# Kernel optimization log

Hardware: AMD Instinct MI355X
Metric: run time of the kernel (lower is better)

Reference implementation:

```python
import jax, jax.numpy as jnp
import numpy as np

V, D, H, L, B = 30000, 128, 4, 128, 512
HD = D // H  # head dim = 32
NL = 2       # num xLSTM layers


def _layernorm(x, w, b):
    mu = x.mean(-1, keepdims=True)
    var = x.var(-1, keepdims=True)
    return (x - mu) * jax.lax.rsqrt(var + 1e-5) * w + b


def _groupnorm_heads(h, w):
    # GroupNorm with num_groups = H over the channel dim (per-head norm), h: [B,L,D]
    hh = h.reshape(h.shape[0], h.shape[1], H, HD)
    mu = hh.mean(-1, keepdims=True)
    var = hh.var(-1, keepdims=True)
    hh = (hh - mu) * jax.lax.rsqrt(var + 1e-5)
    return hh.reshape(h.shape) * w


def _slstm_block(x, W, R, b, gnw, lnw, lnb):
    # x: [B,L,D]; W: [4,D,D] input gate projections (i,f,z,o); R: [4,H,HD,HD] block-diagonal
    # per-head recurrent weights; b: [4,D]; gnw: [D] groupnorm scale.
    bsz = x.shape[0]
    xn = _layernorm(x, lnw, lnb)
    pre = jnp.einsum('bld,god->lbgo', xn, W) + b  # [L,B,4,D]

    def step(carry, pre_t):
        h, c, n, m = carry  # each [B,D]
        rec = jnp.einsum('bhd,ghde->bghe', h.reshape(bsz, H, HD), R).reshape(bsz, 4, D)
        g = pre_t + rec
        it, ft, zt, ot = g[:, 0], g[:, 1], g[:, 2], g[:, 3]
        # stabilized exponential gating (sLSTM vanilla backend)
        m_new = jnp.maximum(ft + m, it)
        i = jnp.exp(it - m_new)
        f = jnp.exp(ft + m - m_new)
        c_new = f * c + i * jnp.tanh(zt)
        n_new = f * n + i
        h_new = jax.nn.sigmoid(ot) * c_new / n_new
        return (h_new, c_new, n_new, m_new), h_new

    z = jnp.zeros((bsz, D), x.dtype)
    _, hs = jax.lax.scan(step, (z, z, z, z), pre)
    hs = jnp.transpose(hs, (1, 0, 2))  # [B,L,D]
    return x + _groupnorm_heads(hs, gnw)  # residual block


def setup_inputs() -> dict:
    key = jax.random.key(0)
    ks = jax.random.split(key, 10)
    s = lambda k, shape, sc: jax.random.normal(k, shape, jnp.float32) * sc
    return {
        'x_ids': jax.random.randint(ks[0], (B, L), 0, V),
        'emb': s(ks[1], (V, D), 0.02),
        'ln_w': jnp.ones((NL, D), jnp.float32),
        'ln_b': jnp.zeros((NL, D), jnp.float32),
        'Wg': s(ks[2], (NL, 4, D, D), 0.05),
        'Rg': s(ks[3], (NL, 4, H, HD, HD), 0.05),
        'bg': s(ks[4], (NL, 4, D), 0.02),
        'gn_w': jnp.ones((NL, D), jnp.float32),
        'w1': s(ks[5], (64, D), 0.05),
        'b1': jnp.zeros((64,), jnp.float32),
        'w2': s(ks[6], (2, 64), 0.05),
        'b2': jnp.zeros((2,), jnp.float32),
    }


def reference(x_ids, emb, ln_w, ln_b, Wg, Rg, bg, gn_w, w1, b1, w2, b2):
    x = emb[x_ids]  # [B,L,D] embedding lookup
    for l in range(NL):
        x = _slstm_block(x, Wg[l], Rg[l], bg[l], gn_w[l], ln_w[l], ln_b[l])
    pooled = x.mean(axis=1)  # mean over sequence, [B,D]
    hid = jax.nn.relu(pooled @ w1.T + b1)  # dropout is identity at eval
    return hid @ w2.T + b2  # [B,2] logits
```

## Files before the change

kernel.cpp:

```cpp
#include <hip/hip_runtime.h>

typedef _Float16 f16;
typedef unsigned int uint;
typedef f16 f16x2 __attribute__((ext_vector_type(2)));
typedef f16 f16x8 __attribute__((ext_vector_type(8)));
typedef __fp16 h16x2 __attribute__((ext_vector_type(2)));
typedef float f32x4 __attribute__((ext_vector_type(4)));

#define Bn 512
#define Ln 128
#define Dn 128
#define Cn 512

__device__ __forceinline__ float fdot2f(uint a, uint b, float c) {
#if __has_builtin(__builtin_amdgcn_fdot2)
  return __builtin_amdgcn_fdot2(__builtin_bit_cast(f16x2, a),
                                __builtin_bit_cast(f16x2, b), c, false);
#else
  f16x2 av = __builtin_bit_cast(f16x2, a), bv = __builtin_bit_cast(f16x2, b);
  return c + (float)av[0] * (float)bv[0] + (float)av[1] * (float)bv[1];
#endif
}

__device__ __forceinline__ uint pk2(float a, float b) {
#if __has_builtin(__builtin_amdgcn_cvt_pkrtz)
  h16x2 v = __builtin_amdgcn_cvt_pkrtz(a, b);
  return __builtin_bit_cast(uint, v);
#else
  f16x2 v; v[0] = (f16)a; v[1] = (f16)b;
  return __builtin_bit_cast(uint, v);
#endif
}

template<int CTRL>
__device__ __forceinline__ float rorf(float x) {
#if __has_builtin(__builtin_amdgcn_mov_dpp)
  int r = __builtin_amdgcn_mov_dpp(__builtin_bit_cast(int, x), CTRL, 0xF, 0xF, true);
  return __builtin_bit_cast(float, r);
#else
  return __shfl_xor(x, (CTRL - 0x120));
#endif
}

__device__ __forceinline__ int swz16i(float x) {
#if __has_builtin(__builtin_amdgcn_ds_swizzle)
  return __builtin_amdgcn_ds_swizzle(__builtin_bit_cast(int, x), 0x401F);
#else
  return __builtin_bit_cast(int, __shfl_xor(x, 16));
#endif
}

__device__ __forceinline__ void read_hu(const f16* base, uint hu[16]) {
  const uint4* hq = (const uint4*)base;
  uint4 q0 = hq[0], q1 = hq[1], q2 = hq[2], q3 = hq[3];
  hu[0]=q0.x; hu[1]=q0.y; hu[2]=q0.z; hu[3]=q0.w;
  hu[4]=q1.x; hu[5]=q1.y; hu[6]=q1.z; hu[7]=q1.w;
  hu[8]=q2.x; hu[9]=q2.y; hu[10]=q2.z; hu[11]=q2.w;
  hu[12]=q3.x; hu[13]=q3.y; hu[14]=q3.z; hu[15]=q3.w;
}

__global__ __launch_bounds__(256) void k_convert(const float* __restrict__ Wg,
                                                 const float* __restrict__ Rg,
                                                 f16* __restrict__ WhF,
                                                 f16* __restrict__ RT) {
  int i = blockIdx.x * 256 + threadIdx.x;
  const int nWfrag = 2 * 4 * 32 * 64;
  if (i < nWfrag) {
    int lane = i & 63;
    int ii   = (i >> 6) & 31;
    int kk   = (i >> 11) & 3;
    int l    = i >> 13;
    int c = ii * 16 + (lane & 15);
    int d = kk * 32 + ((lane >> 4) << 3);
    const float* src = Wg + ((size_t)(l * 512 + c) * 128 + d);
    f16* dst = WhF + (size_t)i * 8;
    #pragma unroll
    for (int j = 0; j < 8; ++j) dst[j] = (f16)src[j];
  } else {
    int j = i - nWfrag;
    if (j < 32768) {
      int dd = j & 31;
      int e  = (j >> 5) & 31;
      int hh = (j >> 10) & 3;
      int g  = (j >> 12) & 3;
      int l  = j >> 14;
      RT[j] = (f16)Rg[((((l * 4 + g) * 4 + hh) * 32 + dd) * 32) + e];
    }
  }
}

template<int EMB>
__global__ __launch_bounds__(256, 2) void k_gemm(const float* __restrict__ xsrc,
                                                 const int* __restrict__ ids,
                                                 const float* __restrict__ lw,
                                                 const float* __restrict__ lb,
                                                 const f16* __restrict__ WhF,
                                                 const float* __restrict__ bias,
                                                 uint2* __restrict__ preP) {
  int w = threadIdx.x >> 6;
  int lane = threadIdx.x & 63;
  int l16 = lane & 15, quad = lane >> 4;

  f16x8 bregs[2][4][4];
  #pragma unroll
  for (int j = 0; j < 2; ++j)
    #pragma unroll
    for (int g = 0; g < 4; ++g) {
      int i = 2 * w + j + 8 * g;
      #pragma unroll
      for (int kk = 0; kk < 4; ++kk)
        bregs[j][g][kk] = *(const f16x8*)(WhF + (size_t)(kk * 32 + i) * 512 + lane * 8);
    }
  float bv[2][4];
  #pragma unroll
  for (int j = 0; j < 2; ++j)
    #pragma unroll
    for (int g = 0; g < 4; ++g)
      bv[j][g] = bias[(2 * w + j + 8 * g) * 16 + l16];

  f32x4 lw4[4][2], lb4[4][2];
  #pragma unroll
  for (int kk = 0; kk < 4; ++kk)
    #pragma unroll
    for (int p = 0; p < 2; ++p) {
      int d0 = kk * 32 + quad * 8 + p * 4;
      lw4[kk][p] = *(const f32x4*)(lw + d0);
      lb4[kk][p] = *(const f32x4*)(lb + d0);
    }

  #pragma unroll 1
  for (int t16 = 0; t16 < 8; ++t16) {
    int m0 = blockIdx.x * 128 + t16 * 16;

    const float* src;
    if (EMB) src = xsrc + (size_t)ids[m0 + l16] * Dn;
    else     src = xsrc + (size_t)(m0 + l16) * Dn;
    const float* sp = src + quad * 8;

    f32x4 v[4][2];
    #pragma unroll
    for (int kk = 0; kk < 4; ++kk) {
      v[kk][0] = *(const f32x4*)(sp + kk * 32);
      v[kk][1] = *(const f32x4*)(sp + kk * 32 + 4);
    }
    float s1 = 0.f, s2 = 0.f;
    #pragma unroll
    for (int kk = 0; kk < 4; ++kk)
      #pragma unroll
      for (int p = 0; p < 2; ++p)
        #pragma unroll
        for (int j = 0; j < 4; ++j) {
          float vv = v[kk][p][j];
          s1 += vv; s2 = fmaf(vv, vv, s2);
        }
    s1 += __shfl_xor(s1, 16);  s2 += __shfl_xor(s2, 16);
    s1 += __shfl_xor(s1, 32);  s2 += __shfl_xor(s2, 32);
    float mu = s1 * (1.f / 128.f);
    float var = s2 * (1.f / 128.f) - mu * mu;
    float rs = rsqrtf(var + 1e-5f);

    f16x8 a[4];
    #pragma unroll
    for (int kk = 0; kk < 4; ++kk)
      #pragma unroll
      for (int p = 0; p < 2; ++p)
        #pragma unroll
        for (int j = 0; j < 4; ++j)
          a[kk][p * 4 + j] = (f16)((v[kk][p][j] - mu) * rs * lw4[kk][p][j] + lb4[kk][p][j]);

    f32x4 acc[2][4] = {};
    #pragma unroll
    for (int kk = 0; kk < 4; ++kk)
      #pragma unroll
      for (int j = 0; j < 2; ++j)
        #pragma unroll
        for (int g = 0; g < 4; ++g)
          acc[j][g] = __builtin_amdgcn_mfma_f32_16x16x32_f16(a[kk], bregs[j][g][kk], acc[j][g], 0, 0, 0);

    #pragma unroll
    for (int r = 0; r < 4; ++r) {
      int m = m0 + quad * 4 + r;
      #pragma unroll
      for (int j = 0; j < 2; ++j) {
        uint2 vv;
        vv.x = pk2(acc[j][0][r] + bv[j][0], acc[j][1][r] + bv[j][1]);
        vv.y = pk2(acc[j][2][r] + bv[j][2], acc[j][3][r] + bv[j][3]);
        preP[(size_t)m * Dn + (2 * w + j) * 16 + l16] = vv;
      }
    }
  }
}

template<int LAST>
__global__ __launch_bounds__(256, 1) void k_scan(const uint2* __restrict__ preP,
                                                 const f16* __restrict__ RT,
                                                 const float* __restrict__ gnw,
                                                 const float* __restrict__ xsrc,
                                                 const int* __restrict__ ids,
                                                 float* __restrict__ xout,
                                                 const float* __restrict__ hw1,
                                                 const float* __restrict__ hb1,
                                                 const float* __restrict__ hw2,
                                                 const float* __restrict__ hb2,
                                                 float* __restrict__ out) {
  const int w = threadIdx.x >> 6;
  const int lane = threadIdx.x & 63;
  const int s = w >> 1;
  const int b = blockIdx.x * 2 + s;
  const int d = ((w & 1) << 6) + lane;
  const int head = d >> 5;
  const int e = d & 31;
  const int half = lane >> 5;

  __shared__ __align__(16) f16 hsh[4][64];
  __shared__ float pool2[2][128];
  __shared__ float hid2[2][64];

  uint rr[4][16];
  const uint* RT32 = (const uint*)RT;
  #pragma unroll
  for (int g = 0; g < 4; ++g) {
    const uint* p = RT32 + ((g * 4 + head) * 32 + e) * 16;
    #pragma unroll
    for (int j = 0; j < 16; ++j) rr[g][j] = p[j];
  }
  const float gw = gnw[d];
  const f16* hbase = &hsh[w][half * 32];

  hsh[w][lane] = (f16)0.f;

  const uint2* pp = preP + (size_t)b * Ln * Dn + d;
  const float* xp = xsrc + (size_t)b * Ln * Dn + d;
  const int*   idr = ids + b * Ln;
  float* xo = xout + (size_t)b * Ln * Dn + d;

  uint2 pb[4]; float xb[4]; int idb[4];
  #pragma unroll
  for (int k = 0; k < 4; ++k) {
    pb[k] = pp[(size_t)k * Dn];
    if (LAST) {
      xb[k] = xp[(size_t)k * Dn];
    } else {
      xb[k] = xsrc[(size_t)idr[k] * Dn + d];
      idb[k] = idr[k + 4];
    }
  }

  uint hu[16];
  read_hu(hbase, hu);

  float cc = 0.f, nc = 0.f, mc = 0.f, psum = 0.f;
  float hprev = 0.f, xprev = 0.f;
  float u1 = 0.f, u2 = 0.f;
  int   w1 = 0,   w2 = 0;

  #pragma unroll 1
  for (int t = 0; t < Ln; t += 4) {
    #pragma unroll
    for (int k = 0; k < 4; ++k) {
      int tt = t + k;
      uint2 pc = pb[k]; float xc = xb[k];
      pb[k] = pp[(size_t)(tt + 4) * Dn];
      if (LAST) {
        xb[k] = xp[(size_t)(tt + 4) * Dn];
      } else {
        xb[k] = xsrc[(size_t)idb[k] * Dn + d];
        int ni = tt + 8;
        idb[k] = idr[ni > 127 ? 127 : ni];
      }

      if (tt > 0) {
        float s1 = u1 + __builtin_bit_cast(float, w1);
        float s2 = u2 + __builtin_bit_cast(float, w2);
        float mu = s1 * (1.f / 32.f);
        float va = s2 * (1.f / 32.f) - mu * mu;
        float ov = xprev + (hprev - mu) * rsqrtf(va + 1e-5f) * gw;
        if (LAST) psum += ov;
        else      xo[(size_t)(tt - 1) * Dn] = ov;
      }

      float a0 = 0.f, a1 = 0.f, a2 = 0.f, a3 = 0.f;
      float c0 = 0.f, c1 = 0.f, c2 = 0.f, c3 = 0.f;
      #pragma unroll
      for (int j = 0; j < 8; ++j) {
        a0 = fdot2f(hu[j], rr[0][j], a0);
        a1 = fdot2f(hu[j], rr[1][j], a1);
        a2 = fdot2f(hu[j], rr[2][j], a2);
        a3 = fdot2f(hu[j], rr[3][j], a3);
        c0 = fdot2f(hu[j + 8], rr[0][j + 8], c0);
        c1 = fdot2f(hu[j + 8], rr[1][j + 8], c1);
        c2 = fdot2f(hu[j + 8], rr[2][j + 8], c2);
        c3 = fdot2f(hu[j + 8], rr[3][j + 8], c3);
      }
      f16x2 lo = __builtin_bit_cast(f16x2, pc.x);
      f16x2 hi = __builtin_bit_cast(f16x2, pc.y);
      float it = ((float)lo[0] + a0) + c0;
      float ft = ((float)lo[1] + a1) + c1;
      float zt = ((float)hi[0] + a2) + c2;
      float ot = ((float)hi[1] + a3) + c3;

      float mn = fmaxf(ft + mc, it);
      float iv = __expf(it - mn);
      float fv = __expf(ft + mc - mn);
      float zc = fminf(fmaxf(zt, -15.f), 15.f);
      float ez = __expf(2.f * zc);
      float tz = (ez - 1.f) * __builtin_amdgcn_rcpf(ez + 1.f);
      float cn = fv * cc + iv * tz;
      float nn = fv * nc + iv;
      float hn = cn * __builtin_amdgcn_rcpf((1.f + __expf(-ot)) * nn);
      cc = cn; nc = nn; mc = mn;

      hsh[w][lane] = (f16)hn;

      float t1v = hn, t2v = hn * hn;
      t1v += rorf<0x121>(t1v);  t2v += rorf<0x121>(t2v);
      t1v += rorf<0x122>(t1v);  t2v += rorf<0x122>(t2v);
      t1v += rorf<0x124>(t1v);  t2v += rorf<0x124>(t2v);
      t1v += rorf<0x128>(t1v);  t2v += rorf<0x128>(t2v);
      w1 = swz16i(t1v);
      w2 = swz16i(t2v);
      u1 = t1v; u2 = t2v;

      read_hu(hbase, hu);

      hprev = hn; xprev = xc;
    }
  }

  {
    float s1 = u1 + __builtin_bit_cast(float, w1);
    float s2 = u2 + __builtin_bit_cast(float, w2);
    float mu = s1 * (1.f / 32.f);
    float va = s2 * (1.f / 32.f) - mu * mu;
    float ov = xprev + (hprev - mu) * rsqrtf(va + 1e-5f) * gw;
    if (LAST) {
      psum += ov;
      pool2[s][d] = psum * (1.f / 128.f);
      __syncthreads();
      if ((w & 1) == 0) {
        int sq = w >> 1;
        float acc = hb1[lane];
        const float* wr = hw1 + (size_t)lane * Dn;
        const float* pl = &pool2[sq][0];
        #pragma unroll 8
        for (int dd = 0; dd < Dn; dd += 4) {
          f32x4 wv = *(const f32x4*)(wr + dd);
          acc += wv[0]*pl[dd] + wv[1]*pl[dd+1] + wv[2]*pl[dd+2] + wv[3]*pl[dd+3];
        }
        hid2[sq][lane] = fmaxf(acc, 0.f);
      }
      __syncthreads();
      if ((w & 1) == 0 && lane < 2) {
        int sq = w >> 1;
        float acc = hb2[lane];
        const float* wr = hw2 + lane * 64;
        #pragma unroll 4
        for (int j = 0; j < 64; ++j) acc += hid2[sq][j] * wr[j];
        out[(blockIdx.x * 2 + sq) * 2 + lane] = acc;
      }
    } else {
      xo[(size_t)(Ln - 1) * Dn] = ov;
    }
  }
}

extern "C" void kernel_launch(void* const* d_in, const int* in_sizes, int n_in,
                              void* d_out, int out_size, void* d_ws, size_t ws_size,
                              hipStream_t stream) {
  const int*   ids  = (const int*)d_in[0];
  const float* emb  = (const float*)d_in[1];
  const float* ln_w = (const float*)d_in[2];
  const float* ln_b = (const float*)d_in[3];
  const float* Wg   = (const float*)d_in[4];
  const float* Rg   = (const float*)d_in[5];
  const float* bg   = (const float*)d_in[6];
  const float* gn_w = (const float*)d_in[7];
  const float* w1   = (const float*)d_in[8];
  const float* b1   = (const float*)d_in[9];
  const float* w2   = (const float*)d_in[10];
  const float* b2   = (const float*)d_in[11];
  float* out = (float*)d_out;

  char* ws = (char*)d_ws;
  uint2* preP = (uint2*)ws;
  float* x1   = (float*)(ws + 67108864);
  f16*   WhF  = (f16*)(ws + 100663296);
  f16*   RT   = (f16*)(ws + 100663296 + 262144);

  k_convert<<<192, 256, 0, stream>>>(Wg, Rg, WhF, RT);

  k_gemm<1><<<512, 256, 0, stream>>>(emb, ids, ln_w, ln_b, WhF, bg, preP);
  k_scan<0><<<256, 256, 0, stream>>>(preP, RT, gn_w, emb, ids, x1,
                                     nullptr, nullptr, nullptr, nullptr, nullptr);
  k_gemm<0><<<512, 256, 0, stream>>>(x1, nullptr, ln_w + Dn, ln_b + Dn,
                                     WhF + 65536, bg + Cn, preP);
  k_scan<1><<<256, 256, 0, stream>>>(preP, RT + 16384, gn_w + Dn, x1, nullptr,
                                     nullptr, w1, b1, w2, b2, out);
}
```

Before: 229.0 us.

## Fuse gate-projection GEMM into sLSTM scan kernel with LDS-chunked producer/consumer waves

```diff
diff --git a/kernel.cpp b/kernel.cpp
--- a/kernel.cpp
+++ b/kernel.cpp
@@ -89,34 +89,24 @@
   }
 }
 
-template<int EMB>
-__global__ __launch_bounds__(256, 2) void k_gemm(const float* __restrict__ xsrc,
-                                                 const int* __restrict__ ids,
-                                                 const float* __restrict__ lw,
-                                                 const float* __restrict__ lb,
-                                                 const f16* __restrict__ WhF,
-                                                 const float* __restrict__ bias,
-                                                 uint2* __restrict__ preP) {
-  int w = threadIdx.x >> 6;
+template<int EMB, int NI>
+__device__ void gemm_chunk(const float* __restrict__ xsrc,
+                           const int* __restrict__ idr,
+                           const float* __restrict__ lw,
+                           const float* __restrict__ lb,
+                           const f16* __restrict__ Wh,
+                           const float* __restrict__ bias,
+                           uint2 (*__restrict__ ldsPb)[128],
+                           int chunk, int i7b) {
   int lane = threadIdx.x & 63;
   int l16 = lane & 15, quad = lane >> 4;
 
-  f16x8 bregs[2][4][4];
+  float bv[NI][4];
   #pragma unroll
-  for (int j = 0; j < 2; ++j)
-    #pragma unroll
-    for (int g = 0; g < 4; ++g) {
-      int i = 2 * w + j + 8 * g;
-      #pragma unroll
-      for (int kk = 0; kk < 4; ++kk)
-        bregs[j][g][kk] = *(const f16x8*)(WhF + (size_t)(kk * 32 + i) * 512 + lane * 8);
-    }
-  float bv[2][4];
-  #pragma unroll
-  for (int j = 0; j < 2; ++j)
+  for (int i = 0; i < NI; ++i)
     #pragma unroll
     for (int g = 0; g < 4; ++g)
-      bv[j][g] = bias[(2 * w + j + 8 * g) * 16 + l16];
+      bv[i][g] = bias[(g * 8 + i7b + i) * 16 + l16];
 
   f32x4 lw4[4][2], lb4[4][2];
   #pragma unroll
@@ -129,13 +119,11 @@
     }
 
   #pragma unroll 1
-  for (int t16 = 0; t16 < 8; ++t16) {
-    int m0 = blockIdx.x * 128 + t16 * 16;
-
-    const float* src;
-    if (EMB) src = xsrc + (size_t)ids[m0 + l16] * Dn;
-    else     src = xsrc + (size_t)(m0 + l16) * Dn;
-    const float* sp = src + quad * 8;
+  for (int h = 0; h < 2; ++h) {
+    int m0loc = chunk * 32 + h * 16;
+    const float* sp;
+    if (EMB) sp = xsrc + (size_t)idr[m0loc + l16] * Dn + quad * 8;
+    else     sp = xsrc + (size_t)(m0loc + l16) * Dn + quad * 8;
 
     f32x4 v[4][2];
     #pragma unroll
@@ -168,198 +156,216 @@
         for (int j = 0; j < 4; ++j)
           a[kk][p * 4 + j] = (f16)((v[kk][p][j] - mu) * rs * lw4[kk][p][j] + lb4[kk][p][j]);
 
-    f32x4 acc[2][4] = {};
+    f32x4 acc[NI][4] = {};
     #pragma unroll
     for (int kk = 0; kk < 4; ++kk)
       #pragma unroll
-      for (int j = 0; j < 2; ++j)
+      for (int i = 0; i < NI; ++i)
         #pragma unroll
-        for (int g = 0; g < 4; ++g)
-          acc[j][g] = __builtin_amdgcn_mfma_f32_16x16x32_f16(a[kk], bregs[j][g][kk], acc[j][g], 0, 0, 0);
+        for (int g = 0; g < 4; ++g) {
+          f16x8 bf = *(const f16x8*)(Wh + (size_t)(kk * 32 + g * 8 + i7b + i) * 512 + lane * 8);
+          acc[i][g] = __builtin_amdgcn_mfma_f32_16x16x32_f16(a[kk], bf, acc[i][g], 0, 0, 0);
+        }
 
     #pragma unroll
     for (int r = 0; r < 4; ++r) {
-      int m = m0 + quad * 4 + r;
+      int rowl = h * 16 + quad * 4 + r;
       #pragma unroll
-      for (int j = 0; j < 2; ++j) {
+      for (int i = 0; i < NI; ++i) {
         uint2 vv;
-        vv.x = pk2(acc[j][0][r] + bv[j][0], acc[j][1][r] + bv[j][1]);
-        vv.y = pk2(acc[j][2][r] + bv[j][2], acc[j][3][r] + bv[j][3]);
-        preP[(size_t)m * Dn + (2 * w + j) * 16 + l16] = vv;
+        vv.x = pk2(acc[i][0][r] + bv[i][0], acc[i][1][r] + bv[i][1]);
+        vv.y = pk2(acc[i][2][r] + bv[i][2], acc[i][3][r] + bv[i][3]);
+        ldsPb[rowl][(i7b + i) * 16 + l16] = vv;
       }
     }
   }
 }
 
 template<int LAST>
-__global__ __launch_bounds__(256, 1) void k_scan(const uint2* __restrict__ preP,
-                                                 const f16* __restrict__ RT,
-                                                 const float* __restrict__ gnw,
-                                                 const float* __restrict__ xsrc,
-                                                 const int* __restrict__ ids,
-                                                 float* __restrict__ xout,
-                                                 const float* __restrict__ hw1,
-                                                 const float* __restrict__ hb1,
-                                                 const float* __restrict__ hw2,
-                                                 const float* __restrict__ hb2,
-                                                 float* __restrict__ out) {
+__global__ __launch_bounds__(256, 2) void k_fused(const int* __restrict__ ids,
+                                                  const float* __restrict__ emb,
+                                                  const float* __restrict__ ln_w,
+                                                  const float* __restrict__ ln_b,
+                                                  const float* __restrict__ bg,
+                                                  const float* __restrict__ gn_w,
+                                                  const float* __restrict__ hw1,
+                                                  const float* __restrict__ hb1,
+                                                  const float* __restrict__ hw2,
+                                                  const float* __restrict__ hb2,
+                                                  const f16* __restrict__ WhF,
+                                                  const f16* __restrict__ RT,
+                                                  float* __restrict__ x1,
+                                                  float* __restrict__ out) {
   const int w = threadIdx.x >> 6;
   const int lane = threadIdx.x & 63;
-  const int s = w >> 1;
-  const int b = blockIdx.x * 2 + s;
-  const int d = ((w & 1) << 6) + lane;
+  const int b = blockIdx.x;
+
+  __shared__ __align__(16) uint2 ldsP[2][32][128];
+  __shared__ __align__(16) f16 hsh[2][64];
+  __shared__ float pool[128];
+  __shared__ float hid[64];
+
+  const float* lw   = ln_w + (LAST ? Dn : 0);
+  const float* lb   = ln_b + (LAST ? Dn : 0);
+  const float* bias = bg + (LAST ? Cn : 0);
+  const f16*   Wh   = WhF + (LAST ? 65536 : 0);
+  const f16*   RTl  = RT + (LAST ? 16384 : 0);
+  const float* gnw  = gn_w + (LAST ? Dn : 0);
+  const float* gsrc = LAST ? (x1 + (size_t)b * Ln * Dn) : emb;
+  const int*   idr  = ids + b * Ln;
+
+  gemm_chunk<LAST ? 0 : 1, 2>(gsrc, idr, lw, lb, Wh, bias, ldsP[0], 0, 2 * w);
+  __syncthreads();
+
+  const int d = (w << 6) + lane;
   const int head = d >> 5;
   const int e = d & 31;
   const int half = lane >> 5;
-
-  __shared__ __align__(16) f16 hsh[4][64];
-  __shared__ float pool2[2][128];
-  __shared__ float hid2[2][64];
-
-  uint rr[4][16];
-  const uint* RT32 = (const uint*)RT;
-  #pragma unroll
-  for (int g = 0; g < 4; ++g) {
-    const uint* p = RT32 + ((g * 4 + head) * 32 + e) * 16;
-    #pragma unroll
-    for (int j = 0; j < 16; ++j) rr[g][j] = p[j];
-  }
-  const float gw = gnw[d];
-  const f16* hbase = &hsh[w][half * 32];
-
-  hsh[w][lane] = (f16)0.f;
-
-  const uint2* pp = preP + (size_t)b * Ln * Dn + d;
-  const float* xp = xsrc + (size_t)b * Ln * Dn + d;
-  const int*   idr = ids + b * Ln;
-  float* xo = xout + (size_t)b * Ln * Dn + d;
-
-  uint2 pb[4]; float xb[4]; int idb[4];
-  #pragma unroll
-  for (int k = 0; k < 4; ++k) {
-    pb[k] = pp[(size_t)k * Dn];
-    if (LAST) {
-      xb[k] = xp[(size_t)k * Dn];
-    } else {
-      xb[k] = xsrc[(size_t)idr[k] * Dn + d];
-      idb[k] = idr[k + 4];
-    }
-  }
-
-  uint hu[16];
-  read_hu(hbase, hu);
-
+  float gw = 0.f;
+  const f16* hbase = &hsh[w & 1][half * 32];
+  const float* xp = x1 + (size_t)b * Ln * Dn + d;
+  float* xo = x1 + (size_t)b * Ln * Dn + d;
+  float xb[4]; int idb[4];
   float cc = 0.f, nc = 0.f, mc = 0.f, psum = 0.f;
   float hprev = 0.f, xprev = 0.f;
   float u1 = 0.f, u2 = 0.f;
   int   w1 = 0,   w2 = 0;
 
+  if (w < 2) {
+    gw = gnw[d];
+    hsh[w][lane] = (f16)0.f;
+    #pragma unroll
+    for (int k = 0; k < 4; ++k) {
+      if (LAST) { xb[k] = xp[(size_t)k * Dn]; idb[k] = 0; }
+      else      { xb[k] = emb[(size_t)idr[k] * Dn + d]; idb[k] = idr[k + 4]; }
+    }
+  }
+
   #pragma unroll 1
-  for (int t = 0; t < Ln; t += 4) {
-    #pragma unroll
-    for (int k = 0; k < 4; ++k) {
-      int tt = t + k;
-      uint2 pc = pb[k]; float xc = xb[k];
-      pb[k] = pp[(size_t)(tt + 4) * Dn];
-      if (LAST) {
-        xb[k] = xp[(size_t)(tt + 4) * Dn];
-      } else {
-        xb[k] = xsrc[(size_t)idb[k] * Dn + d];
-        int ni = tt + 8;
-        idb[k] = idr[ni > 127 ? 127 : ni];
+  for (int c = 0; c < 4; ++c) {
+    if (w < 2) {
+      uint rr[4][16];
+      const uint* RT32 = (const uint*)RTl;
+      #pragma unroll
+      for (int g = 0; g < 4; ++g) {
+        const uint* p = RT32 + ((g * 4 + head) * 32 + e) * 16;
+        #pragma unroll
+        for (int j = 0; j < 16; ++j) rr[g][j] = p[j];
       }
-
-      if (tt > 0) {
-        float s1 = u1 + __builtin_bit_cast(float, w1);
-        float s2 = u2 + __builtin_bit_cast(float, w2);
-        float mu = s1 * (1.f / 32.f);
-        float va = s2 * (1.f / 32.f) - mu * mu;
-        float ov = xprev + (hprev - mu) * rsqrtf(va + 1e-5f) * gw;
-        if (LAST) psum += ov;
-        else      xo[(size_t)(tt - 1) * Dn] = ov;
+      uint hu[16];
+      read_hu(hbase, hu);
+      const uint2* Pc = &ldsP[c & 1][0][0];
+      uint2 pcn = Pc[d];
+
+      #pragma unroll 1
+      for (int t8 = 0; t8 < 8; ++t8) {
+        #pragma unroll
+        for (int k = 0; k < 4; ++k) {
+          int s = t8 * 4 + k;
+          int tt = c * 32 + s;
+          uint2 pc = pcn;
+          if (s < 31) pcn = Pc[(s + 1) * 128 + d];
+          float xc = xb[k];
+          if (LAST) {
+            xb[k] = xp[(size_t)(tt + 4) * Dn];
+          } else {
+            xb[k] = emb[(size_t)idb[k] * Dn + d];
+            int ni = tt + 8;
+            idb[k] = idr[ni > 127 ? 127 : ni];
+          }
+
+          if (tt > 0) {
+            float s1 = u1 + __builtin_bit_cast(float, w1);
+            float s2 = u2 + __builtin_bit_cast(float, w2);
+            float mu = s1 * (1.f / 32.f);
+            float va = s2 * (1.f / 32.f) - mu * mu;
+            float ov = xprev + (hprev - mu) * rsqrtf(va + 1e-5f) * gw;
+            if (LAST) psum += ov;
+            else      xo[(size_t)(tt - 1) * Dn] = ov;
+          }
+
+          float a0 = 0.f, a1 = 0.f, a2 = 0.f, a3 = 0.f;
+          float c0 = 0.f, c1 = 0.f, c2 = 0.f, c3 = 0.f;
+          #pragma unroll
+          for (int j = 0; j < 8; ++j) {
+            a0 = fdot2f(hu[j], rr[0][j], a0);
+            a1 = fdot2f(hu[j], rr[1][j], a1);
+            a2 = fdot2f(hu[j], rr[2][j], a2);
+            a3 = fdot2f(hu[j], rr[3][j], a3);
+            c0 = fdot2f(hu[j + 8], rr[0][j + 8], c0);
+            c1 = fdot2f(hu[j + 8], rr[1][j + 8], c1);
+            c2 = fdot2f(hu[j + 8], rr[2][j + 8], c2);
+            c3 = fdot2f(hu[j + 8], rr[3][j + 8], c3);
+          }
+          f16x2 lo = __builtin_bit_cast(f16x2, pc.x);
+          f16x2 hi = __builtin_bit_cast(f16x2, pc.y);
+          float it = ((float)lo[0] + a0) + c0;
+          float ft = ((float)lo[1] + a1) + c1;
+          float zt = ((float)hi[0] + a2) + c2;
+          float ot = ((float)hi[1] + a3) + c3;
+
+          float mn = fmaxf(ft + mc, it);
+          float iv = __expf(it - mn);
+          float fv = __expf(ft + mc - mn);
+          float zc = fminf(fmaxf(zt, -15.f), 15.f);
+          float ez = __expf(2.f * zc);
+          float tz = (ez - 1.f) * __builtin_amdgcn_rcpf(ez + 1.f);
+          float cn = fv * cc + iv * tz;
+          float nn = fv * nc + iv;
+          float hn = cn * __builtin_amdgcn_rcpf((1.f + __expf(-ot)) * nn);
+          cc = cn; nc = nn; mc = mn;
+
+          hsh[w][lane] = (f16)hn;
+
+          float t1v = hn, t2v = hn * hn;
+          t1v += rorf<0x121>(t1v);  t2v += rorf<0x121>(t2v);
+          t1v += rorf<0x122>(t1v);  t2v += rorf<0x122>(t2v);
+          t1v += rorf<0x124>(t1v);  t2v += rorf<0x124>(t2v);
+          t1v += rorf<0x128>(t1v);  t2v += rorf<0x128>(t2v);
+          w1 = swz16i(t1v);
+          w2 = swz16i(t2v);
+          u1 = t1v; u2 = t2v;
+
+          read_hu(hbase, hu);
+
+          hprev = hn; xprev = xc;
+        }
       }
-
-      float a0 = 0.f, a1 = 0.f, a2 = 0.f, a3 = 0.f;
-      float c0 = 0.f, c1 = 0.f, c2 = 0.f, c3 = 0.f;
-      #pragma unroll
-      for (int j = 0; j < 8; ++j) {
-        a0 = fdot2f(hu[j], rr[0][j], a0);
-        a1 = fdot2f(hu[j], rr[1][j], a1);
-        a2 = fdot2f(hu[j], rr[2][j], a2);
-        a3 = fdot2f(hu[j], rr[3][j], a3);
-        c0 = fdot2f(hu[j + 8], rr[0][j + 8], c0);
-        c1 = fdot2f(hu[j + 8], rr[1][j + 8], c1);
-        c2 = fdot2f(hu[j + 8], rr[2][j + 8], c2);
-        c3 = fdot2f(hu[j + 8], rr[3][j + 8], c3);
-      }
-      f16x2 lo = __builtin_bit_cast(f16x2, pc.x);
-      f16x2 hi = __builtin_bit_cast(f16x2, pc.y);
-      float it = ((float)lo[0] + a0) + c0;
-      float ft = ((float)lo[1] + a1) + c1;
-      float zt = ((float)hi[0] + a2) + c2;
-      float ot = ((float)hi[1] + a3) + c3;
-
-      float mn = fmaxf(ft + mc, it);
-      float iv = __expf(it - mn);
-      float fv = __expf(ft + mc - mn);
-      float zc = fminf(fmaxf(zt, -15.f), 15.f);
-      float ez = __expf(2.f * zc);
-      float tz = (ez - 1.f) * __builtin_amdgcn_rcpf(ez + 1.f);
-      float cn = fv * cc + iv * tz;
-      float nn = fv * nc + iv;
-      float hn = cn * __builtin_amdgcn_rcpf((1.f + __expf(-ot)) * nn);
-      cc = cn; nc = nn; mc = mn;
-
-      hsh[w][lane] = (f16)hn;
-
-      float t1v = hn, t2v = hn * hn;
-      t1v += rorf<0x121>(t1v);  t2v += rorf<0x121>(t2v);
-      t1v += rorf<0x122>(t1v);  t2v += rorf<0x122>(t2v);
-      t1v += rorf<0x124>(t1v);  t2v += rorf<0x124>(t2v);
-      t1v += rorf<0x128>(t1v);  t2v += rorf<0x128>(t2v);
-      w1 = swz16i(t1v);
-      w2 = swz16i(t2v);
-      u1 = t1v; u2 = t2v;
-
-      read_hu(hbase, hu);
-
-      hprev = hn; xprev = xc;
-    }
-  }
-
-  {
+    } else if (c < 3) {
+      gemm_chunk<LAST ? 0 : 1, 4>(gsrc, idr, lw, lb, Wh, bias,
+                                  ldsP[(c + 1) & 1], c + 1, (w - 2) * 4);
+    }
+    __syncthreads();
+  }
+
+  if (w < 2) {
     float s1 = u1 + __builtin_bit_cast(float, w1);
     float s2 = u2 + __builtin_bit_cast(float, w2);
     float mu = s1 * (1.f / 32.f);
     float va = s2 * (1.f / 32.f) - mu * mu;
     float ov = xprev + (hprev - mu) * rsqrtf(va + 1e-5f) * gw;
-    if (LAST) {
-      psum += ov;
-      pool2[s][d] = psum * (1.f / 128.f);
-      __syncthreads();
-      if ((w & 1) == 0) {
-        int sq = w >> 1;
-        float acc = hb1[lane];
-        const float* wr = hw1 + (size_t)lane * Dn;
-        const float* pl = &pool2[sq][0];
-        #pragma unroll 8
-        for (int dd = 0; dd < Dn; dd += 4) {
-          f32x4 wv = *(const f32x4*)(wr + dd);
-          acc += wv[0]*pl[dd] + wv[1]*pl[dd+1] + wv[2]*pl[dd+2] + wv[3]*pl[dd+3];
-        }
-        hid2[sq][lane] = fmaxf(acc, 0.f);
+    if (LAST) { psum += ov; pool[d] = psum * (1.f / 128.f); }
+    else      xo[(size_t)(Ln - 1) * Dn] = ov;
+  }
+  if (LAST) {
+    __syncthreads();
+    if (w == 0) {
+      float acc = hb1[lane];
+      const float* wr = hw1 + (size_t)lane * Dn;
+      #pragma unroll 8
+      for (int dd = 0; dd < Dn; dd += 4) {
+        f32x4 wv = *(const f32x4*)(wr + dd);
+        acc += wv[0]*pool[dd] + wv[1]*pool[dd+1] + wv[2]*pool[dd+2] + wv[3]*pool[dd+3];
       }
-      __syncthreads();
-      if ((w & 1) == 0 && lane < 2) {
-        int sq = w >> 1;
-        float acc = hb2[lane];
-        const float* wr = hw2 + lane * 64;
-        #pragma unroll 4
-        for (int j = 0; j < 64; ++j) acc += hid2[sq][j] * wr[j];
-        out[(blockIdx.x * 2 + sq) * 2 + lane] = acc;
-      }
-    } else {
-      xo[(size_t)(Ln - 1) * Dn] = ov;
+      hid[lane] = fmaxf(acc, 0.f);
+    }
+    __syncthreads();
+    if (w == 0 && lane < 2) {
+      float acc = hb2[lane];
+      const float* wr = hw2 + lane * 64;
+      #pragma unroll 4
+      for (int j = 0; j < 64; ++j) acc += hid[j] * wr[j];
+      out[b * 2 + lane] = acc;
     }
   }
 }
@@ -382,18 +388,14 @@
   float* out = (float*)d_out;
 
   char* ws = (char*)d_ws;
-  uint2* preP = (uint2*)ws;
-  float* x1   = (float*)(ws + 67108864);
-  f16*   WhF  = (f16*)(ws + 100663296);
-  f16*   RT   = (f16*)(ws + 100663296 + 262144);
+  float* x1  = (float*)ws;
+  f16*   WhF = (f16*)(ws + 33554432);
+  f16*   RT  = (f16*)(ws + 33554432 + 262144);
 
   k_convert<<<192, 256, 0, stream>>>(Wg, Rg, WhF, RT);
 
-  k_gemm<1><<<512, 256, 0, stream>>>(emb, ids, ln_w, ln_b, WhF, bg, preP);
-  k_scan<0><<<256, 256, 0, stream>>>(preP, RT, gn_w, emb, ids, x1,
-                                     nullptr, nullptr, nullptr, nullptr, nullptr);
-  k_gemm<0><<<512, 256, 0, stream>>>(x1, nullptr, ln_w + Dn, ln_b + Dn,
-                                     WhF + 65536, bg + Cn, preP);
-  k_scan<1><<<256, 256, 0, stream>>>(preP, RT + 16384, gn_w + Dn, x1, nullptr,
-                                     nullptr, w1, b1, w2, b2, out);
-}
+  k_fused<0><<<512, 256, 0, stream>>>(ids, emb, ln_w, ln_b, bg, gn_w,
+                                      w1, b1, w2, b2, WhF, RT, x1, out);
+  k_fused<1><<<512, 256, 0, stream>>>(ids, emb, ln_w, ln_b, bg, gn_w,
+                                      w1, b1, w2, b2, WhF, RT, x1, out);
+}
```

Result: slower. 563.5 us (+146.1%).
